# Optimization experiments

Hardware: AMD Instinct MI355X
Metric: run time of the kernel (lower is better)

Reference implementation:

```python
import jax, jax.numpy as jnp
import numpy as np

N_WORDS, MAX_LEN = 16384, 16
VOCAB, EMB, HID = 128, 64, 256


def setup_inputs() -> dict:
    key = jax.random.key(0)
    ks = jax.random.split(key, 11)
    s = 1.0 / np.sqrt(HID)  # torch LSTMCell default init scale
    u = lambda k, shape: jax.random.uniform(k, shape, jnp.float32, -s, s)
    return {
        "char_ids": jax.random.randint(ks[0], (N_WORDS, MAX_LEN), 0, VOCAB, dtype=jnp.int32),
        "lengths": jax.random.randint(ks[1], (N_WORDS,), 1, MAX_LEN + 1, dtype=jnp.int32),
        "emb": jax.random.normal(ks[2], (VOCAB, EMB), jnp.float32),
        "W_ih_f": u(ks[3], (4 * HID, EMB)),
        "W_hh_f": u(ks[4], (4 * HID, HID)),
        "b_ih_f": u(ks[5], (4 * HID,)),
        "b_hh_f": u(ks[6], (4 * HID,)),
        "W_ih_b": u(ks[7], (4 * HID, EMB)),
        "W_hh_b": u(ks[8], (4 * HID, HID)),
        "b_ih_b": u(ks[9], (4 * HID,)),
        "b_hh_b": u(ks[10], (4 * HID,)),
    }


def _run_lstm(xs, mask, W_ih, W_hh, b):
    # xs: [T, N, E]; mask: [T, N]; returns final masked hidden state [N, H]
    n = xs.shape[1]
    h0 = jnp.zeros((n, W_hh.shape[1]), xs.dtype)

    def step(carry, inp):
        h, c = carry
        x, m = inp
        gates = x @ W_ih.T + h @ W_hh.T + b  # [N, 4H], torch gate order i,f,g,o
        i, f, g, o = jnp.split(gates, 4, axis=-1)
        c2 = jax.nn.sigmoid(f) * c + jax.nn.sigmoid(i) * jnp.tanh(g)
        h2 = jax.nn.sigmoid(o) * jnp.tanh(c2)
        m = m[:, None]
        return (jnp.where(m, h2, h), jnp.where(m, c2, c)), None

    (h, _), _ = jax.lax.scan(step, (h0, h0), (xs, mask))
    return h


def reference(char_ids, lengths, emb, W_ih_f, W_hh_f, b_ih_f, b_hh_f,
              W_ih_b, W_hh_b, b_ih_b, b_hh_b):
    x = emb[char_ids]                                   # [N, T, E]
    t = jnp.arange(MAX_LEN)
    mask = t[None, :] < lengths[:, None]                # [N, T] valid chars
    xs = x.transpose(1, 0, 2)                           # [T, N, E]
    ms = mask.T                                         # [T, N]
    h_f = _run_lstm(xs, ms, W_ih_f, W_hh_f, b_ih_f + b_hh_f)
    # per-word reversed sequence: chars processed from last to first
    ridx = jnp.clip(lengths[:, None] - 1 - t[None, :], 0)  # [N, T]
    xr = jnp.take_along_axis(x, ridx[:, :, None], axis=1)  # [N, T, E]
    h_b = _run_lstm(xr.transpose(1, 0, 2), ms, W_ih_b, W_hh_b, b_ih_b + b_hh_b)
    return jnp.concatenate([h_f, h_b], axis=-1)         # [N, 2H]
```

## Files before the change

### kernel.cpp

```cpp
#include <hip/hip_runtime.h>

#define N_WORDS 16384
#define MAXL    16
#define VOCABSZ 128
#define EMBD    64
#define HID     256
#define GATES   1024
#define KTOT    320
#define AROW    328
#define M_TILE  64
#define NT      256

typedef __attribute__((ext_vector_type(8))) short bf16x8;
typedef __attribute__((ext_vector_type(4))) float f32x4;
typedef __attribute__((ext_vector_type(4))) int   i32x4;

#define OFF_WSW   0ul
#define OFF_EMB   1310720ul
#define OFF_BIAS  1327104ul
#define OFF_SORT  1335296ul
#define OFF_HIST  1400832ul
#define OFF_BASE  1400896ul
#define OFF_CNT   1400960ul

__device__ inline short tobf(float f) {
  unsigned u = __float_as_uint(f);
  unsigned r = (u + 0x7fffu + ((u >> 16) & 1u)) >> 16;
  return (short)r;
}
__device__ inline float aexp2(float x) { float r; asm("v_exp_f32 %0, %1" : "=v"(r) : "v"(x)); return r; }
__device__ inline float arcp(float x)  { float r; asm("v_rcp_f32 %0, %1" : "=v"(r) : "v"(x)); return r; }
__device__ inline float fsig(float x)   { return arcp(1.0f + aexp2(x * -1.4426950408889634f)); }
__device__ inline float ftanhf(float x) { return 1.0f - 2.0f * arcp(1.0f + aexp2(x * 2.8853900817779268f)); }

__global__ void prep_w(const float* __restrict__ Wihf, const float* __restrict__ Whhf,
                       const float* __restrict__ Wihb, const float* __restrict__ Whhb,
                       short* __restrict__ wsw) {
  int id = blockIdx.x * 256 + threadIdx.x;
  if (id >= 81920) return;
  int d    = id / 40960;
  int r    = id % 40960;
  int R    = r / 640;
  int r2   = r % 640;
  int kk   = r2 / 64;
  int lane = r2 % 64;
  int m    = lane & 15;
  int unit = R * 4 + (m >> 2);
  int ty   = m & 3;
  int g    = ty * 256 + unit;
  int kb   = kk * 32 + (lane >> 4) * 8;
  const float* Wih = d ? Wihb : Wihf;
  const float* Whh = d ? Whhb : Whhf;
  bf16x8 v;
#pragma unroll
  for (int j = 0; j < 8; ++j) {
    int k = kb + j;
    float f = (k < HID) ? Whh[g * HID + k] : Wih[g * EMBD + (k - HID)];
    v[j] = tobf(f);
  }
  ((bf16x8*)wsw)[id] = v;
}

__global__ void prep_misc(const float* __restrict__ emb,
                          const float* __restrict__ bihf, const float* __restrict__ bhhf,
                          const float* __restrict__ bihb, const float* __restrict__ bhhb,
                          short* __restrict__ embw, float* __restrict__ biasg) {
  int id = blockIdx.x * 256 + threadIdx.x;
  if (id < VOCABSZ * EMBD) {
    embw[id] = tobf(emb[id]);
  } else {
    int r = id - VOCABSZ * EMBD;
    if (r < 2048) {
      int d = r >> 10, n = r & 1023;
      int g = (n & 3) * 256 + (n >> 2);
      biasg[r] = d ? (bihb[g] + bhhb[g]) : (bihf[g] + bhhf[g]);
    }
  }
}

__global__ void k_hist(const int* __restrict__ lengths, int* __restrict__ hist) {
  int id = blockIdx.x * 256 + threadIdx.x;
  if (id < N_WORDS) atomicAdd(&hist[lengths[id] - 1], 1);
}
__global__ void k_scan(const int* __restrict__ hist, int* __restrict__ basep) {
  if (threadIdx.x == 0 && blockIdx.x == 0) {
    int s = 0;
    for (int i = 0; i < 16; ++i) { basep[i] = s; s += hist[i]; }
  }
}
__global__ void k_scat(const int* __restrict__ lengths, const int* __restrict__ basep,
                       int* __restrict__ cnt, int* __restrict__ sorted) {
  int id = blockIdx.x * 256 + threadIdx.x;
  if (id < N_WORDS) {
    int b = lengths[id] - 1;
    int p = basep[b] + atomicAdd(&cnt[b], 1);
    sorted[p] = id;
  }
}

__global__ __launch_bounds__(512, 1) void lstm_main(
    const int* __restrict__ char_ids, const int* __restrict__ lengths,
    const short* __restrict__ wsw, const short* __restrict__ embw,
    const float* __restrict__ biasg, const int* __restrict__ sorted,
    float* __restrict__ out) {
  __shared__ __align__(16) short A[M_TILE * AROW];
  __shared__ __align__(16) int   charl[M_TILE * 16];
  __shared__ __align__(16) float biasl[GATES];
  __shared__ __align__(16) f32x4 c4[8 * 8 * 64];
  __shared__ int lenl[M_TILE];
  __shared__ int swl[M_TILE];

  const int tid  = threadIdx.x;
  const int lane = tid & 63;
  const int wv   = tid >> 6;
  const int quad = lane >> 4;
  const int colc = lane & 15;
  const int pb   = blockIdx.x;
  const int dir  = pb & 1;
  const int qb   = pb >> 1;
  const int tile = (qb & 1) ? (255 - (qb >> 1)) : (qb >> 1);

  if (tid < M_TILE) {
    int sw = sorted[tile * M_TILE + tid];
    swl[tid]  = sw;
    lenl[tid] = lengths[sw];
  }
  if (tid < 256) ((f32x4*)biasl)[tid] = ((const f32x4*)(biasg + dir * GATES))[tid];
  for (int i = tid; i < M_TILE * AROW / 2; i += 512) ((int*)A)[i] = 0;
  for (int i = tid; i < 8 * 8 * 64; i += 512) c4[i] = (f32x4){0.f, 0.f, 0.f, 0.f};
  __syncthreads();

  if (tid < 256) {
    int w = tid >> 2, ch = tid & 3;
    ((i32x4*)charl)[tid] = ((const i32x4*)(char_ids + swl[w] * 16))[ch];
  }
  int Lmax = lenl[lane];
  for (int o = 32; o; o >>= 1) { int v = __shfl_xor(Lmax, o, 64); Lmax = Lmax > v ? Lmax : v; }
  __syncthreads();

  auto gather_x = [&](int tt) {
    int wl = wv * 8 + (lane >> 3);
    int part = lane & 7;
    int lw = lenl[wl];
    int pos = (dir == 0) ? tt : (lw - 1 - tt);
    pos = pos < 0 ? 0 : (pos > 15 ? 15 : pos);
    int cid = charl[wl * 16 + pos];
    bf16x8 e = *(const bf16x8*)(embw + cid * EMBD + part * 8);
    *(bf16x8*)(A + wl * AROW + HID + part * 8) = e;
  };
  gather_x(0);

  int lenw[4], hadrb[4], oadr[4];
#pragma unroll
  for (int ct = 0; ct < 4; ++ct) {
    int wl = ct * 16 + colc;
    lenw[ct]  = lenl[wl];
    hadrb[ct] = wl * AROW + 32 * wv + quad;
    oadr[ct]  = swl[wl] * 512 + dir * 256 + 32 * wv + quad;
  }
  const short* wp = wsw + ((size_t)dir * 64 + wv * 8) * 10 * 64 * 8 + lane * 8;
  f32x4* cptr = c4 + wv * (8 * 64) + lane;

  __syncthreads();

  bf16x8 wA[10], wB[10];
#pragma unroll
  for (int kk = 0; kk < 10; ++kk) wA[kk] = *(const bf16x8*)(wp + kk * 512);

#pragma unroll 1
  for (int t = 0; t < Lmax; ++t) {
    bf16x8 hx[4][10];
#pragma unroll
    for (int ct = 0; ct < 4; ++ct)
#pragma unroll
      for (int kk = 0; kk < 10; ++kk)
        hx[ct][kk] = *(const bf16x8*)(A + (ct * 16 + colc) * AROW + kk * 32 + quad * 8);

    __syncthreads();

    auto wtile = [&](int rt, bf16x8(&wc)[10], bf16x8(&wn)[10], int pre) {
#pragma unroll
      for (int kk = 0; kk < 10; ++kk) wn[kk] = *(const bf16x8*)(wp + (pre * 10 + kk) * 512);
      f32x4 co4 = cptr[rt * 64];
      f32x4 bias4 = *(const f32x4*)(biasl + 128 * wv + 16 * rt + 4 * quad);
      f32x4 acc[4];
#pragma unroll
      for (int ct = 0; ct < 4; ++ct) acc[ct] = bias4;
#pragma unroll
      for (int kk = 0; kk < 10; ++kk)
#pragma unroll
        for (int ct = 0; ct < 4; ++ct)
          acc[ct] = __builtin_amdgcn_mfma_f32_16x16x32_bf16(wc[kk], hx[ct][kk], acc[ct], 0, 0, 0);

      f32x4 cnew;
#pragma unroll
      for (int ct = 0; ct < 4; ++ct) {
        float ig = fsig(acc[ct][0]);
        float fg = fsig(acc[ct][1]);
        float gg = ftanhf(acc[ct][2]);
        float og = fsig(acc[ct][3]);
        float co_v = co4[ct];
        float c2 = fg * co_v + ig * gg;
        float h2 = og * ftanhf(c2);
        bool act = t < lenw[ct];
        cnew[ct] = act ? c2 : co_v;
        if (act) A[hadrb[ct] + 4 * rt] = tobf(h2);
        if (t == lenw[ct] - 1) out[oadr[ct] + 4 * rt] = h2;
      }
      cptr[rt * 64] = cnew;
    };

#pragma unroll 1
    for (int rt2 = 0; rt2 < 8; rt2 += 2) {
      wtile(rt2,     wA, wB, rt2 + 1);
      wtile(rt2 + 1, wB, wA, (rt2 + 2) & 7);
    }

    gather_x(t + 1);
    __syncthreads();
  }
}

extern "C" void kernel_launch(void* const* d_in, const int* in_sizes, int n_in,
                              void* d_out, int out_size, void* d_ws, size_t ws_size,
                              hipStream_t stream) {
  const int*   char_ids = (const int*)d_in[0];
  const int*   lengths  = (const int*)d_in[1];
  const float* emb      = (const float*)d_in[2];
  const float* Wihf     = (const float*)d_in[3];
  const float* Whhf     = (const float*)d_in[4];
  const float* bihf     = (const float*)d_in[5];
  const float* bhhf     = (const float*)d_in[6];
  const float* Wihb     = (const float*)d_in[7];
  const float* Whhb     = (const float*)d_in[8];
  const float* bihb     = (const float*)d_in[9];
  const float* bhhb     = (const float*)d_in[10];

  char* ws = (char*)d_ws;
  short* wsw   = (short*)(ws + OFF_WSW);
  short* embw  = (short*)(ws + OFF_EMB);
  float* biasg = (float*)(ws + OFF_BIAS);
  int*   sortd = (int*)(ws + OFF_SORT);
  int*   hist  = (int*)(ws + OFF_HIST);
  int*   basep = (int*)(ws + OFF_BASE);
  int*   cnt   = (int*)(ws + OFF_CNT);

  hipMemsetAsync(hist, 0, 192, stream);
  k_hist<<<64, 256, 0, stream>>>(lengths, hist);
  k_scan<<<1, 64, 0, stream>>>(hist, basep);
  k_scat<<<64, 256, 0, stream>>>(lengths, basep, cnt, sortd);
  prep_w<<<320, 256, 0, stream>>>(Wihf, Whhf, Wihb, Whhb, wsw);
  prep_misc<<<40, 256, 0, stream>>>(emb, bihf, bhhf, bihb, bhhb, embw, biasg);
  lstm_main<<<512, 512, 0, stream>>>(char_ids, lengths, wsw, embw, biasg, sortd,
                                     (float*)d_out);
}
```

Measured before the change: 485.0 us.

## Software-pipeline gate MFMA with previous tile's epilogue and prefetch embeddings early

Restructures the per-timestep loop so the MFMA work for tile rt runs ahead of the sigmoid/tanh epilogue for tile rt-1, using two alternating accumulator sets. Weight double-buffering is replaced by a single weight register set loaded right after each MFMA tile, which frees registers. The embedding gather for the next step is issued before the barrier, held in registers and stored late. MFMA sections also raise wave priority with s_setprio. Precomputed per-column address arrays are dropped to save registers, at the cost of recomputing addresses and reading swl from LDS in the epilogue. The intent is to overlap transcendental ALU work and global loads with matrix work, but loading weights into the same registers just consumed may expose global-load latency.

```diff
diff --git a/kernel.cpp b/kernel.cpp
--- a/kernel.cpp
+++ b/kernel.cpp
@@ -138,85 +138,94 @@
   for (int o = 32; o; o >>= 1) { int v = __shfl_xor(Lmax, o, 64); Lmax = Lmax > v ? Lmax : v; }
   __syncthreads();
 
-  auto gather_x = [&](int tt) {
-    int wl = wv * 8 + (lane >> 3);
-    int part = lane & 7;
-    int lw = lenl[wl];
+  const int xwl   = wv * 8 + (lane >> 3);
+  const int xpart = lane & 7;
+  auto x_load = [&](int tt) -> bf16x8 {
+    int lw = lenl[xwl];
     int pos = (dir == 0) ? tt : (lw - 1 - tt);
     pos = pos < 0 ? 0 : (pos > 15 ? 15 : pos);
-    int cid = charl[wl * 16 + pos];
-    bf16x8 e = *(const bf16x8*)(embw + cid * EMBD + part * 8);
-    *(bf16x8*)(A + wl * AROW + HID + part * 8) = e;
-  };
-  gather_x(0);
-
-  int lenw[4], hadrb[4], oadr[4];
-#pragma unroll
-  for (int ct = 0; ct < 4; ++ct) {
-    int wl = ct * 16 + colc;
-    lenw[ct]  = lenl[wl];
-    hadrb[ct] = wl * AROW + 32 * wv + quad;
-    oadr[ct]  = swl[wl] * 512 + dir * 256 + 32 * wv + quad;
-  }
+    int cid = charl[xwl * 16 + pos];
+    return *(const bf16x8*)(embw + cid * EMBD + xpart * 8);
+  };
+  auto x_store = [&](bf16x8 e) {
+    *(bf16x8*)(A + xwl * AROW + HID + xpart * 8) = e;
+  };
+  x_store(x_load(0));
+
+  int lenw[4];
+#pragma unroll
+  for (int ct = 0; ct < 4; ++ct) lenw[ct] = lenl[ct * 16 + colc];
+  const int h0    = colc * AROW + 32 * wv + quad;
+  const int obase = dir * 256 + 32 * wv + quad;
   const short* wp = wsw + ((size_t)dir * 64 + wv * 8) * 10 * 64 * 8 + lane * 8;
   f32x4* cptr = c4 + wv * (8 * 64) + lane;
 
   __syncthreads();
 
-  bf16x8 wA[10], wB[10];
-#pragma unroll
-  for (int kk = 0; kk < 10; ++kk) wA[kk] = *(const bf16x8*)(wp + kk * 512);
+  bf16x8 wc[10];
+  bf16x8 hx[4][10];
+
+  auto ldw = [&](int rt) {
+#pragma unroll
+    for (int kk = 0; kk < 10; ++kk) wc[kk] = *(const bf16x8*)(wp + (rt * 10 + kk) * 512);
+  };
+  auto mfma_tile = [&](int rt, f32x4 (&acc)[4]) {
+    f32x4 b4 = *(const f32x4*)(biasl + 128 * wv + 16 * rt + 4 * quad);
+#pragma unroll
+    for (int ct = 0; ct < 4; ++ct) acc[ct] = b4;
+    __builtin_amdgcn_s_setprio(1);
+#pragma unroll
+    for (int kk = 0; kk < 10; ++kk)
+#pragma unroll
+      for (int ct = 0; ct < 4; ++ct)
+        acc[ct] = __builtin_amdgcn_mfma_f32_16x16x32_bf16(wc[kk], hx[ct][kk], acc[ct], 0, 0, 0);
+    __builtin_amdgcn_s_setprio(0);
+  };
+  auto epi_tile = [&](int t, int rt, f32x4 (&acc)[4]) {
+    f32x4 co4 = cptr[rt * 64];
+    f32x4 cnew;
+#pragma unroll
+    for (int ct = 0; ct < 4; ++ct) {
+      float ig = fsig(acc[ct][0]);
+      float fg = fsig(acc[ct][1]);
+      float gg = ftanhf(acc[ct][2]);
+      float og = fsig(acc[ct][3]);
+      float co_v = co4[ct];
+      float c2 = fg * co_v + ig * gg;
+      float h2 = og * ftanhf(c2);
+      bool act = t < lenw[ct];
+      cnew[ct] = act ? c2 : co_v;
+      if (act) A[h0 + ct * 5248 + 4 * rt] = tobf(h2);
+      if (t == lenw[ct] - 1) {
+        int sw = swl[ct * 16 + colc];
+        out[(size_t)sw * 512 + obase + 4 * rt] = h2;
+      }
+    }
+    cptr[rt * 64] = cnew;
+  };
 
 #pragma unroll 1
   for (int t = 0; t < Lmax; ++t) {
-    bf16x8 hx[4][10];
 #pragma unroll
     for (int ct = 0; ct < 4; ++ct)
 #pragma unroll
       for (int kk = 0; kk < 10; ++kk)
         hx[ct][kk] = *(const bf16x8*)(A + (ct * 16 + colc) * AROW + kk * 32 + quad * 8);
-
+    bf16x8 e = x_load(t + 1);
+    ldw(0);
     __syncthreads();
 
-    auto wtile = [&](int rt, bf16x8(&wc)[10], bf16x8(&wn)[10], int pre) {
-#pragma unroll
-      for (int kk = 0; kk < 10; ++kk) wn[kk] = *(const bf16x8*)(wp + (pre * 10 + kk) * 512);
-      f32x4 co4 = cptr[rt * 64];
-      f32x4 bias4 = *(const f32x4*)(biasl + 128 * wv + 16 * rt + 4 * quad);
-      f32x4 acc[4];
-#pragma unroll
-      for (int ct = 0; ct < 4; ++ct) acc[ct] = bias4;
-#pragma unroll
-      for (int kk = 0; kk < 10; ++kk)
-#pragma unroll
-        for (int ct = 0; ct < 4; ++ct)
-          acc[ct] = __builtin_amdgcn_mfma_f32_16x16x32_bf16(wc[kk], hx[ct][kk], acc[ct], 0, 0, 0);
-
-      f32x4 cnew;
-#pragma unroll
-      for (int ct = 0; ct < 4; ++ct) {
-        float ig = fsig(acc[ct][0]);
-        float fg = fsig(acc[ct][1]);
-        float gg = ftanhf(acc[ct][2]);
-        float og = fsig(acc[ct][3]);
-        float co_v = co4[ct];
-        float c2 = fg * co_v + ig * gg;
-        float h2 = og * ftanhf(c2);
-        bool act = t < lenw[ct];
-        cnew[ct] = act ? c2 : co_v;
-        if (act) A[hadrb[ct] + 4 * rt] = tobf(h2);
-        if (t == lenw[ct] - 1) out[oadr[ct] + 4 * rt] = h2;
-      }
-      cptr[rt * 64] = cnew;
-    };
-
-#pragma unroll 1
-    for (int rt2 = 0; rt2 < 8; rt2 += 2) {
-      wtile(rt2,     wA, wB, rt2 + 1);
-      wtile(rt2 + 1, wB, wA, (rt2 + 2) & 7);
-    }
-
-    gather_x(t + 1);
+    f32x4 accP[4], accQ[4];
+    mfma_tile(0, accP); ldw(1);
+    mfma_tile(1, accQ); ldw(2); epi_tile(t, 0, accP);
+    mfma_tile(2, accP); ldw(3); epi_tile(t, 1, accQ);
+    mfma_tile(3, accQ); ldw(4); epi_tile(t, 2, accP);
+    mfma_tile(4, accP); ldw(5); epi_tile(t, 3, accQ);
+    mfma_tile(5, accQ); ldw(6); epi_tile(t, 4, accP);
+    mfma_tile(6, accP); ldw(7); epi_tile(t, 5, accQ);
+    mfma_tile(7, accQ);         epi_tile(t, 6, accP);
+    x_store(e);
+    epi_tile(t, 7, accQ);
     __syncthreads();
   }
 }
```

Result: slower. 1.136 ms (+134.3%).
